# Optimization experiments

Hardware: AMD Instinct MI355X
Metric: run time of the kernel (lower is better)

The kernel has to match this reference:

```python
import jax, jax.numpy as jnp
import numpy as np

D_MODEL = 1024
N_HEADS = 16
D_HEAD = 64
BATCH = 4
SEQ = 2048
NEG = -1000000000.0


def setup_inputs() -> dict:
    key = jax.random.key(0)
    k1, k2, k3, k4, k5 = jax.random.split(key, 5)
    x = jax.random.normal(k1, (BATCH, SEQ, D_MODEL), dtype=jnp.float32)
    std = 0.02
    wq = jax.random.normal(k2, (N_HEADS, D_HEAD, D_MODEL), dtype=jnp.float32) * std
    wk = jax.random.normal(k3, (N_HEADS, D_HEAD, D_MODEL), dtype=jnp.float32) * std
    wv = jax.random.normal(k4, (N_HEADS, D_HEAD, D_MODEL), dtype=jnp.float32) * std
    wo = jax.random.normal(k5, (D_MODEL, N_HEADS * D_HEAD), dtype=jnp.float32) * std
    return {"x": x, "wq": wq, "wk": wk, "wv": wv, "wo": wo}


def reference(x, wq, wk, wv, wo):
    # x: [b, s, d_model]; wq/wk/wv: [h, d_head, d_model]; wo: [d_model, h*d_head]
    b, s, _ = x.shape
    scale = jnp.sqrt(jnp.asarray(D_HEAD, x.dtype))
    q = jnp.einsum('bsd,hed->bhse', x, wq)
    k = jnp.einsum('bsd,hed->bhse', x, wk)
    v = jnp.einsum('bsd,hed->bhse', x, wv)
    scores = jnp.einsum('bhse,bhte->bhst', q, k) / scale
    causal_mask = jnp.triu(jnp.ones((s, s), dtype=bool), k=1)
    scores = jnp.where(causal_mask, jnp.asarray(NEG, scores.dtype), scores)
    weights = jax.nn.softmax(scores, axis=-1)
    heads = jnp.einsum('bhst,bhte->bhse', weights, v)  # [b, h, s, d_head]
    concat = heads.transpose(0, 2, 1, 3).reshape(b, s, N_HEADS * D_HEAD)
    return concat @ wo.T
```

## Files before the change

kernel.cpp:

```cpp
#include <hip/hip_runtime.h>


#define DEV __device__ __forceinline__

typedef __attribute__((ext_vector_type(8))) __bf16 bf16x8;
typedef __attribute__((ext_vector_type(4))) float f32x4;
typedef unsigned short u16;

struct alignas(8) U16x4 { u16 x, y, z, w; };

DEV u16 f2bf(float f) {
  unsigned int u = __builtin_bit_cast(unsigned int, f);
  u = u + 0x7FFFu + ((u >> 16) & 1u);
  return (u16)(u >> 16);
}

DEV unsigned cvt_pk_bf16(float a, float b) {
  unsigned r;
  asm("v_cvt_pk_bf16_f32 %0, %1, %2" : "=v"(r) : "v"(a), "v"(b));
  return r;
}

DEV f32x4 mfma16(uint2 a, uint2 b, f32x4 c) {
  f32x4 d;
  asm("v_mfma_f32_16x16x16_bf16 %0, %1, %2, %3" : "=v"(d) : "v"(a), "v"(b), "v"(c));
  return d;
}

DEV void gload_lds16(const void* g, void* l) {
  __builtin_amdgcn_global_load_lds(
      (const __attribute__((address_space(1))) unsigned int*)g,
      (__attribute__((address_space(3))) unsigned int*)l, 16, 0, 0);
}

__global__ __launch_bounds__(256) void cast_all_kernel(
    const float* __restrict__ x, const float* __restrict__ wq,
    const float* __restrict__ wk, const float* __restrict__ wv,
    const float* __restrict__ wo, u16* __restrict__ xb,
    u16* __restrict__ wqkvb, u16* __restrict__ wob) {
  const int i = blockIdx.x * blockDim.x + threadIdx.x;
  const float* src;
  U16x4* dst;
  if (i < 2097152) {
    src = x + (size_t)i * 4;
    dst = reinterpret_cast<U16x4*>(xb) + i;
  } else if (i < 2883584) {
    const int j = i - 2097152;
    const int sel = j >> 18;
    const float* s = sel == 0 ? wq : sel == 1 ? wk : wv;
    src = s + (size_t)(j & 262143) * 4;
    dst = reinterpret_cast<U16x4*>(wqkvb) + j;
  } else {
    const int j = i - 2883584;
    src = wo + (size_t)j * 4;
    dst = reinterpret_cast<U16x4*>(wob) + j;
  }
  const float4 v = *reinterpret_cast<const float4*>(src);
  *dst = U16x4{f2bf(v.x), f2bf(v.y), f2bf(v.z), f2bf(v.w)};
}

template <int MODE, int NBN, bool SBUF>
__global__ __launch_bounds__(256, SBUF ? 3 : 2) void gemm_bt(
    const u16* __restrict__ A, const u16* __restrict__ B,
    void* __restrict__ C0, u16* __restrict__ vtp, int N) {
  constexpr int K = 1024;
  const int d = blockIdx.x;
  const int chunk = gridDim.x >> 3;
  const int vg = (d & 7) * chunk + (d >> 3);
  const int bn = vg % NBN, bm = vg / NBN;
  const int tid = threadIdx.x;
  const int w = tid >> 6, lane = tid & 63, lo = lane & 15, hi = lane >> 4;
  const int wm = w >> 1, wn = w & 1;

  __shared__ char lds[SBUF ? 32768 : 65536];
  char* sA = lds;
  char* sB = lds + (SBUF ? 16384 : 32768);

  const u16* Ag = A + (size_t)(bm * 128) * K;
  const u16* Bg = B + (size_t)(bn * 128) * K;

  f32x4 acc[4][4] = {};

  auto stage = [&](int buf, int k0) {
#pragma unroll
    for (int it = 0; it < 4; ++it) {
      const int L = (it * 4 + w) * 64 + lane;
      const int r = L >> 3, p = L & 7, c = p ^ (r & 7);
      gload_lds16(Ag + (size_t)r * K + k0 + c * 8, sA + buf * 16384 + (it * 4 + w) * 1024);
      gload_lds16(Bg + (size_t)r * K + k0 + c * 8, sB + buf * 16384 + (it * 4 + w) * 1024);
    }
  };
  auto compute = [&](int buf) {
#pragma unroll
    for (int kc = 0; kc < 2; ++kc) {
      bf16x8 af[4], bfr[4];
#pragma unroll
      for (int m = 0; m < 4; ++m) {
        const int r = wm * 64 + m * 16 + lo;
        const int p = (kc * 4 + hi) ^ (r & 7);
        af[m] = *reinterpret_cast<const bf16x8*>(sA + buf * 16384 + r * 128 + p * 16);
      }
#pragma unroll
      for (int n = 0; n < 4; ++n) {
        const int r = wn * 64 + n * 16 + lo;
        const int p = (kc * 4 + hi) ^ (r & 7);
        bfr[n] = *reinterpret_cast<const bf16x8*>(sB + buf * 16384 + r * 128 + p * 16);
      }
#pragma unroll
      for (int m = 0; m < 4; ++m)
#pragma unroll
        for (int n = 0; n < 4; ++n)
          acc[m][n] = __builtin_amdgcn_mfma_f32_16x16x32_bf16(af[m], bfr[n], acc[m][n], 0, 0, 0);
    }
  };

  if constexpr (SBUF) {
    for (int t = 0; t < 16; ++t) {
      stage(0, t * 64);
      __syncthreads();
      compute(0);
      __syncthreads();
    }
  } else {
    stage(0, 0);
    __syncthreads();
    int cur = 0;
    for (int t = 0; t < 16; ++t) {
      if (t + 1 < 16) stage(cur ^ 1, (t + 1) * 64);
      compute(cur);
      __syncthreads();
      cur ^= 1;
    }
  }

  const int colW = bn * 128 + wn * 64;
  const int rowW = bm * 128 + wm * 64;
  if (MODE == 0) {
    float* C = (float*)C0;
#pragma unroll
    for (int m = 0; m < 4; ++m)
#pragma unroll
      for (int n = 0; n < 4; ++n) {
        const int col = colW + n * 16 + lo;
        const int rb = rowW + m * 16 + hi * 4;
#pragma unroll
        for (int rg = 0; rg < 4; ++rg)
          C[(size_t)(rb + rg) * N + col] = acc[m][n][rg];
      }
  } else {
    u16* qkvp = (u16*)C0;
    if (bn * 128 < 2048) {
      const float qs = (bn < 8) ? 0.18033688011112042f : 1.0f;
#pragma unroll
      for (int m = 0; m < 4; ++m)
#pragma unroll
        for (int n = 0; n < 4; ++n) {
          const int col = colW + n * 16 + lo;
          const int rb = rowW + m * 16 + hi * 4;
#pragma unroll
          for (int rg = 0; rg < 4; ++rg)
            qkvp[(size_t)(rb + rg) * 2048 + col] = f2bf(acc[m][n][rg] * qs);
        }
    } else {
#pragma unroll
      for (int m = 0; m < 4; ++m)
#pragma unroll
        for (int n = 0; n < 4; ++n) {
          const int col = colW + n * 16 + lo;
          const int idx = col - 2048;
          const int hh = idx >> 6, e = idx & 63;
          const int rb = rowW + m * 16 + hi * 4;
          const int bb = rb >> 11, s = rb & 2047;
          U16x4 v4{f2bf(acc[m][n][0]), f2bf(acc[m][n][1]),
                   f2bf(acc[m][n][2]), f2bf(acc[m][n][3])};
          *reinterpret_cast<U16x4*>(vtp + ((size_t)((bb * 16 + hh) * 64 + e)) * 2048 + s) = v4;
        }
    }
  }
}

__global__ __launch_bounds__(512, 4) void attn_kernel(
    const u16* __restrict__ qkv, const u16* __restrict__ vt, u16* __restrict__ heads) {
  const int dd = blockIdx.x;
  const int vg = (dd & 7) * 64 + (dd >> 3);
  const int bx = vg & 7, bh = vg >> 3;
  const int b = bh >> 4, h = bh & 15;
  const int tid = threadIdx.x;
  const int w = tid >> 6, lane = tid & 63, lo = lane & 15, hi = lane >> 4;

  __shared__ char lds[81920];
  char* sQP = lds;
  char* sK  = lds + 16384;
  char* sV  = lds + 49152;

  const u16* Kg = qkv + (size_t)(b * 2048) * 2048 + 1024 + h * 64;
  const u16* Vg = vt + (size_t)bh * 64 * 2048;

  const int kr = tid >> 3, kc_ = (tid & 7) ^ (kr & 7);
  const int vr = tid >> 4, vc_ = (tid & 15) ^ (vr & 7);
  auto stageKV = [&](int buf, int kv0) {
#pragma unroll
    for (int it = 0; it < 2; ++it) {
      gload_lds16(Kg + (size_t)(kv0 + it * 64 + kr) * 2048 + kc_ * 8,
                  sK + buf * 16384 + it * 8192 + w * 1024);
      gload_lds16(Vg + (size_t)(it * 32 + vr) * 2048 + kv0 + vc_ * 8,
                  sV + buf * 16384 + it * 8192 + w * 1024);
    }
  };

  const int qloc = w * 16 + lo;

  for (int rep = 0; rep < 2; ++rep) {
    const int qt = rep ? (15 - bx) : bx;
    const u16* Qg = qkv + (size_t)(b * 2048 + qt * 128) * 2048 + h * 64;

#pragma unroll
    for (int it = 0; it < 2; ++it)
      gload_lds16(Qg + (size_t)(it * 64 + kr) * 2048 + kc_ * 8, sQP + it * 8192 + w * 1024);
    stageKV(0, 0);
    __syncthreads();

    bf16x8 qf[2];
#pragma unroll
    for (int kc = 0; kc < 2; ++kc) {
      const int p = (kc * 4 + hi) ^ (lo & 7);
      qf[kc] = *reinterpret_cast<const bf16x8*>(sQP + qloc * 128 + p * 16);
    }

    f32x4 lvec = {};
    f32x4 oacc[4] = {};

    const int nt = qt + 1;

    auto step = [&](int t, int cur) {
      if (t + 1 < nt) stageKV(cur ^ 1, (t + 1) * 128);
      f32x4 sa[8] = {};
      __builtin_amdgcn_s_setprio(1);
#pragma unroll
      for (int kc = 0; kc < 2; ++kc) {
#pragma unroll
        for (int n = 0; n < 8; ++n) {
          const int r = n * 16 + lo;
          const int p = (kc * 4 + hi) ^ (lo & 7);
          const bf16x8 kf = *reinterpret_cast<const bf16x8*>(sK + cur * 16384 + r * 128 + p * 16);
          sa[n] = __builtin_amdgcn_mfma_f32_16x16x32_bf16(kf, qf[kc], sa[n], 0, 0, 0);
        }
      }
      __builtin_amdgcn_s_setprio(0);

      if (t == nt - 1) {
#pragma unroll
        for (int n = 0; n < 8; ++n)
#pragma unroll
          for (int rg = 0; rg < 4; ++rg)
            if (n * 16 + hi * 4 + rg > qloc) sa[n][rg] = -1e9f;
      }

#pragma unroll
      for (int n = 0; n < 8; ++n)
#pragma unroll
        for (int rg = 0; rg < 4; ++rg) sa[n][rg] = exp2f(sa[n][rg]);
      lvec += ((sa[0] + sa[1]) + (sa[2] + sa[3])) + ((sa[4] + sa[5]) + (sa[6] + sa[7]));

      __builtin_amdgcn_s_setprio(1);
#pragma unroll
      for (int n = 0; n < 8; ++n) {
        const uint2 pb{cvt_pk_bf16(sa[n][0], sa[n][1]), cvt_pk_bf16(sa[n][2], sa[n][3])};
        const int sb = (((2 * n + (hi >> 1)) ^ (lo & 7)) << 4) + ((hi & 1) << 3);
#pragma unroll
        for (int ne = 0; ne < 4; ++ne) {
          const uint2 vf = *reinterpret_cast<const uint2*>(
              sV + cur * 16384 + (ne * 16 + lo) * 256 + sb);
          oacc[ne] = mfma16(vf, pb, oacc[ne]);
        }
      }
      __builtin_amdgcn_s_setprio(0);
      __syncthreads();
    };

    for (int i = 0; i < nt; i += 2) {
      step(i, 0);
      if (i + 1 < nt) step(i + 1, 1);
    }

    float lsum = (lvec[0] + lvec[1]) + (lvec[2] + lvec[3]);
    lsum += __shfl_xor(lsum, 16);
    lsum += __shfl_xor(lsum, 32);
    const float inv = 1.0f / lsum;
    const int q = qt * 128 + qloc;
    u16* dst = heads + (size_t)(b * 2048 + q) * 1024 + h * 64;
#pragma unroll
    for (int ne = 0; ne < 4; ++ne) {
      const unsigned r0 = cvt_pk_bf16(oacc[ne][0] * inv, oacc[ne][1] * inv);
      const unsigned r1 = cvt_pk_bf16(oacc[ne][2] * inv, oacc[ne][3] * inv);
      *reinterpret_cast<uint2*>(dst + ne * 16 + hi * 4) = uint2{r0, r1};
    }
  }
}

extern "C" void kernel_launch(void* const* d_in, const int* in_sizes, int n_in,
                              void* d_out, int out_size, void* d_ws, size_t ws_size,
                              hipStream_t stream) {
  const float* x  = (const float*)d_in[0];
  const float* wq = (const float*)d_in[1];
  const float* wk = (const float*)d_in[2];
  const float* wv = (const float*)d_in[3];
  const float* wo = (const float*)d_in[4];

  char* ws = (char*)d_ws;
  u16* xb    = (u16*)(ws);
  u16* wqkvb = (u16*)(ws + 16777216);
  u16* wob   = (u16*)(ws + 23068672);
  u16* qkv   = (u16*)(ws + 25165824);
  u16* vtp   = (u16*)(ws + 58720256);
  u16* heads = (u16*)(ws + 75497472);

  cast_all_kernel<<<12288, 256, 0, stream>>>(x, wq, wk, wv, wo, xb, wqkvb, wob);

  gemm_bt<1, 24, true><<<1536, 256, 0, stream>>>(xb, wqkvb, qkv, vtp, 3072);
  attn_kernel<<<512, 512, 0, stream>>>(qkv, vtp, heads);
  gemm_bt<0, 8, false><<<512, 256, 0, stream>>>(heads, wob, d_out, nullptr, 1024);
}
```

Before: 168.4 us.

## Restructure attention to 4 waves with 32 query rows each and 64-key tiles

The attention kernel goes from 8 waves of 16 query rows to 4 waves of 32 query rows, so each K/V fragment read from LDS feeds two MFMAs. KV tiles shrink from 128 to 64 keys, which cuts LDS to 48KB and lets each wave skip fully masked causal tiles. This lowers LDS read traffic per FLOP and wasted masked compute, at the cost of more registers per wave, fewer threads per block and twice as many barrier-separated steps.

After: 175.9 us. 4.5% more time.

```diff
diff --git a/kernel.cpp b/kernel.cpp
--- a/kernel.cpp
+++ b/kernel.cpp
@@ -179,7 +179,7 @@
   }
 }
 
-__global__ __launch_bounds__(512, 4) void attn_kernel(
+__global__ __launch_bounds__(256, 3) void attn_kernel(
     const u16* __restrict__ qkv, const u16* __restrict__ vt, u16* __restrict__ heads) {
   const int dd = blockIdx.x;
   const int vg = (dd & 7) * 64 + (dd >> 3);
@@ -188,112 +188,132 @@
   const int tid = threadIdx.x;
   const int w = tid >> 6, lane = tid & 63, lo = lane & 15, hi = lane >> 4;
 
-  __shared__ char lds[81920];
-  char* sQP = lds;
-  char* sK  = lds + 16384;
-  char* sV  = lds + 49152;
+  __shared__ char lds[49152];
+  char* sQ = lds;
+  char* sK = lds + 16384;
+  char* sV = lds + 32768;
 
   const u16* Kg = qkv + (size_t)(b * 2048) * 2048 + 1024 + h * 64;
   const u16* Vg = vt + (size_t)bh * 64 * 2048;
 
-  const int kr = tid >> 3, kc_ = (tid & 7) ^ (kr & 7);
-  const int vr = tid >> 4, vc_ = (tid & 15) ^ (vr & 7);
+  const int sr = lane >> 3, sc = (lane & 7) ^ (lane >> 3);
   auto stageKV = [&](int buf, int kv0) {
 #pragma unroll
-    for (int it = 0; it < 2; ++it) {
-      gload_lds16(Kg + (size_t)(kv0 + it * 64 + kr) * 2048 + kc_ * 8,
-                  sK + buf * 16384 + it * 8192 + w * 1024);
-      gload_lds16(Vg + (size_t)(it * 32 + vr) * 2048 + kv0 + vc_ * 8,
-                  sV + buf * 16384 + it * 8192 + w * 1024);
+    for (int rnd = 0; rnd < 2; ++rnd) {
+      const int r = rnd * 32 + w * 8 + sr;
+      gload_lds16(Kg + (size_t)(kv0 + r) * 2048 + sc * 8, sK + buf * 8192 + rnd * 4096 + w * 1024);
+      gload_lds16(Vg + (size_t)r * 2048 + kv0 + sc * 8, sV + buf * 8192 + rnd * 4096 + w * 1024);
     }
   };
 
-  const int qloc = w * 16 + lo;
+  const int qw = w * 32;
 
   for (int rep = 0; rep < 2; ++rep) {
     const int qt = rep ? (15 - bx) : bx;
     const u16* Qg = qkv + (size_t)(b * 2048 + qt * 128) * 2048 + h * 64;
 
 #pragma unroll
-    for (int it = 0; it < 2; ++it)
-      gload_lds16(Qg + (size_t)(it * 64 + kr) * 2048 + kc_ * 8, sQP + it * 8192 + w * 1024);
+    for (int it = 0; it < 4; ++it) {
+      const int r = it * 32 + w * 8 + sr;
+      gload_lds16(Qg + (size_t)r * 2048 + sc * 8, sQ + it * 4096 + w * 1024);
+    }
     stageKV(0, 0);
     __syncthreads();
 
-    bf16x8 qf[2];
-#pragma unroll
-    for (int kc = 0; kc < 2; ++kc) {
-      const int p = (kc * 4 + hi) ^ (lo & 7);
-      qf[kc] = *reinterpret_cast<const bf16x8*>(sQP + qloc * 128 + p * 16);
-    }
-
-    f32x4 lvec = {};
-    f32x4 oacc[4] = {};
-
-    const int nt = qt + 1;
+    bf16x8 qf[2][2];
+#pragma unroll
+    for (int qg = 0; qg < 2; ++qg)
+#pragma unroll
+      for (int kc = 0; kc < 2; ++kc) {
+        const int r = qw + qg * 16 + lo;
+        const int p = (kc * 4 + hi) ^ (lo & 7);
+        qf[qg][kc] = *reinterpret_cast<const bf16x8*>(sQ + r * 128 + p * 16);
+      }
+
+    f32x4 lvec[2] = {};
+    f32x4 oacc[2][4] = {};
+
+    const int nt = 2 * (qt + 1);
+    const int qmaxw = qt * 128 + qw + 31;
 
     auto step = [&](int t, int cur) {
-      if (t + 1 < nt) stageKV(cur ^ 1, (t + 1) * 128);
-      f32x4 sa[8] = {};
-      __builtin_amdgcn_s_setprio(1);
-#pragma unroll
-      for (int kc = 0; kc < 2; ++kc) {
-#pragma unroll
-        for (int n = 0; n < 8; ++n) {
-          const int r = n * 16 + lo;
-          const int p = (kc * 4 + hi) ^ (lo & 7);
-          const bf16x8 kf = *reinterpret_cast<const bf16x8*>(sK + cur * 16384 + r * 128 + p * 16);
-          sa[n] = __builtin_amdgcn_mfma_f32_16x16x32_bf16(kf, qf[kc], sa[n], 0, 0, 0);
-        }
-      }
-      __builtin_amdgcn_s_setprio(0);
-
-      if (t == nt - 1) {
-#pragma unroll
-        for (int n = 0; n < 8; ++n)
-#pragma unroll
-          for (int rg = 0; rg < 4; ++rg)
-            if (n * 16 + hi * 4 + rg > qloc) sa[n][rg] = -1e9f;
-      }
-
-#pragma unroll
-      for (int n = 0; n < 8; ++n)
-#pragma unroll
-        for (int rg = 0; rg < 4; ++rg) sa[n][rg] = exp2f(sa[n][rg]);
-      lvec += ((sa[0] + sa[1]) + (sa[2] + sa[3])) + ((sa[4] + sa[5]) + (sa[6] + sa[7]));
-
-      __builtin_amdgcn_s_setprio(1);
-#pragma unroll
-      for (int n = 0; n < 8; ++n) {
-        const uint2 pb{cvt_pk_bf16(sa[n][0], sa[n][1]), cvt_pk_bf16(sa[n][2], sa[n][3])};
-        const int sb = (((2 * n + (hi >> 1)) ^ (lo & 7)) << 4) + ((hi & 1) << 3);
-#pragma unroll
-        for (int ne = 0; ne < 4; ++ne) {
-          const uint2 vf = *reinterpret_cast<const uint2*>(
-              sV + cur * 16384 + (ne * 16 + lo) * 256 + sb);
-          oacc[ne] = mfma16(vf, pb, oacc[ne]);
-        }
-      }
-      __builtin_amdgcn_s_setprio(0);
+      if (t + 1 < nt) stageKV(cur ^ 1, (t + 1) * 64);
+      if (t * 64 <= qmaxw) {
+        f32x4 sa[2][4] = {};
+        __builtin_amdgcn_s_setprio(1);
+#pragma unroll
+        for (int kc = 0; kc < 2; ++kc) {
+#pragma unroll
+          for (int n = 0; n < 4; ++n) {
+            const int r = n * 16 + lo;
+            const int p = (kc * 4 + hi) ^ (lo & 7);
+            const bf16x8 kf = *reinterpret_cast<const bf16x8*>(sK + cur * 8192 + r * 128 + p * 16);
+            sa[0][n] = __builtin_amdgcn_mfma_f32_16x16x32_bf16(kf, qf[0][kc], sa[0][n], 0, 0, 0);
+            sa[1][n] = __builtin_amdgcn_mfma_f32_16x16x32_bf16(kf, qf[1][kc], sa[1][n], 0, 0, 0);
+          }
+        }
+        __builtin_amdgcn_s_setprio(0);
+
+        if (t >= nt - 2) {
+          const int kb = t * 64 - qt * 128;
+#pragma unroll
+          for (int qg = 0; qg < 2; ++qg) {
+            const int thr = qw + qg * 16 + lo - kb;
+#pragma unroll
+            for (int n = 0; n < 4; ++n)
+#pragma unroll
+              for (int rg = 0; rg < 4; ++rg)
+                if (n * 16 + hi * 4 + rg > thr) sa[qg][n][rg] = -1e9f;
+          }
+        }
+
+#pragma unroll
+        for (int qg = 0; qg < 2; ++qg) {
+#pragma unroll
+          for (int n = 0; n < 4; ++n)
+#pragma unroll
+            for (int rg = 0; rg < 4; ++rg) sa[qg][n][rg] = exp2f(sa[qg][n][rg]);
+          lvec[qg] += (sa[qg][0] + sa[qg][1]) + (sa[qg][2] + sa[qg][3]);
+        }
+
+        __builtin_amdgcn_s_setprio(1);
+#pragma unroll
+        for (int n = 0; n < 4; ++n) {
+          const uint2 pb0{cvt_pk_bf16(sa[0][n][0], sa[0][n][1]), cvt_pk_bf16(sa[0][n][2], sa[0][n][3])};
+          const uint2 pb1{cvt_pk_bf16(sa[1][n][0], sa[1][n][1]), cvt_pk_bf16(sa[1][n][2], sa[1][n][3])};
+          const int sb = (((2 * n + (hi >> 1)) ^ (lo & 7)) << 4) + ((hi & 1) << 3);
+#pragma unroll
+          for (int ne = 0; ne < 4; ++ne) {
+            const uint2 vf = *reinterpret_cast<const uint2*>(
+                sV + cur * 8192 + (ne * 16 + lo) * 128 + sb);
+            oacc[0][ne] = mfma16(vf, pb0, oacc[0][ne]);
+            oacc[1][ne] = mfma16(vf, pb1, oacc[1][ne]);
+          }
+        }
+        __builtin_amdgcn_s_setprio(0);
+      }
       __syncthreads();
     };
 
     for (int i = 0; i < nt; i += 2) {
       step(i, 0);
-      if (i + 1 < nt) step(i + 1, 1);
-    }
-
-    float lsum = (lvec[0] + lvec[1]) + (lvec[2] + lvec[3]);
-    lsum += __shfl_xor(lsum, 16);
-    lsum += __shfl_xor(lsum, 32);
-    const float inv = 1.0f / lsum;
-    const int q = qt * 128 + qloc;
-    u16* dst = heads + (size_t)(b * 2048 + q) * 1024 + h * 64;
-#pragma unroll
-    for (int ne = 0; ne < 4; ++ne) {
-      const unsigned r0 = cvt_pk_bf16(oacc[ne][0] * inv, oacc[ne][1] * inv);
-      const unsigned r1 = cvt_pk_bf16(oacc[ne][2] * inv, oacc[ne][3] * inv);
-      *reinterpret_cast<uint2*>(dst + ne * 16 + hi * 4) = uint2{r0, r1};
+      step(i + 1, 1);
+    }
+
+#pragma unroll
+    for (int qg = 0; qg < 2; ++qg) {
+      float lsum = (lvec[qg][0] + lvec[qg][1]) + (lvec[qg][2] + lvec[qg][3]);
+      lsum += __shfl_xor(lsum, 16);
+      lsum += __shfl_xor(lsum, 32);
+      const float inv = 1.0f / lsum;
+      const int q = qt * 128 + qw + qg * 16 + lo;
+      u16* dst = heads + (size_t)(b * 2048 + q) * 1024 + h * 64;
+#pragma unroll
+      for (int ne = 0; ne < 4; ++ne) {
+        const unsigned r0 = cvt_pk_bf16(oacc[qg][ne][0] * inv, oacc[qg][ne][1] * inv);
+        const unsigned r1 = cvt_pk_bf16(oacc[qg][ne][2] * inv, oacc[qg][ne][3] * inv);
+        *reinterpret_cast<uint2*>(dst + ne * 16 + hi * 4) = uint2{r0, r1};
+      }
     }
   }
 }
@@ -318,6 +338,6 @@
   cast_all_kernel<<<12288, 256, 0, stream>>>(x, wq, wk, wv, wo, xb, wqkvb, wob);
 
   gemm_bt<1, 24, true><<<1536, 256, 0, stream>>>(xb, wqkvb, qkv, vtp, 3072);
-  attn_kernel<<<512, 512, 0, stream>>>(qkv, vtp, heads);
+  attn_kernel<<<512, 256, 0, stream>>>(qkv, vtp, heads);
   gemm_bt<0, 8, false><<<512, 256, 0, stream>>>(heads, wob, d_out, nullptr, 1024);
 }
```

## Replace GEMM LDS staging with 4-deep K=32 ring buffer pipeline

Applied to the files above, without the earlier changes.

The GEMM kernel now stages 128x32 A/B tiles into a 4-slot LDS ring, prefetching three slices ahead. Explicit vmcnt waits and raw s_barrier replace __syncthreads, and MFMA issue gets raised priority. This replaces the single-buffer K=64 loop used by the QKV projection and the double buffer used by the output projection. The goal is to hide global-to-LDS latency behind MFMA work, at the cost of more barriers per K step and 64KB of LDS, which limits occupancy to 2 blocks.

Measured after the change: 169.6 us. Within noise of the previous version (+0.7%).

```diff
diff --git a/kernel.cpp b/kernel.cpp
--- a/kernel.cpp
+++ b/kernel.cpp
@@ -31,6 +31,13 @@
   __builtin_amdgcn_global_load_lds(
       (const __attribute__((address_space(1))) unsigned int*)g,
       (__attribute__((address_space(3))) unsigned int*)l, 16, 0, 0);
+}
+
+DEV void waitvm(int n) {
+  if (n >= 12)     asm volatile("s_waitcnt vmcnt(12)" ::: "memory");
+  else if (n == 8) asm volatile("s_waitcnt vmcnt(8)" ::: "memory");
+  else if (n == 4) asm volatile("s_waitcnt vmcnt(4)" ::: "memory");
+  else             asm volatile("s_waitcnt vmcnt(0)" ::: "memory");
 }
 
 __global__ __launch_bounds__(256) void cast_all_kernel(
@@ -59,8 +66,8 @@
   *dst = U16x4{f2bf(v.x), f2bf(v.y), f2bf(v.z), f2bf(v.w)};
 }
 
-template <int MODE, int NBN, bool SBUF>
-__global__ __launch_bounds__(256, SBUF ? 3 : 2) void gemm_bt(
+template <int MODE, int NBN>
+__global__ __launch_bounds__(256, 2) void gemm_bt(
     const u16* __restrict__ A, const u16* __restrict__ B,
     void* __restrict__ C0, u16* __restrict__ vtp, int N) {
   constexpr int K = 1024;
@@ -72,65 +79,57 @@
   const int w = tid >> 6, lane = tid & 63, lo = lane & 15, hi = lane >> 4;
   const int wm = w >> 1, wn = w & 1;
 
-  __shared__ char lds[SBUF ? 32768 : 65536];
-  char* sA = lds;
-  char* sB = lds + (SBUF ? 16384 : 32768);
+  __shared__ char lds[65536];
 
   const u16* Ag = A + (size_t)(bm * 128) * K;
   const u16* Bg = B + (size_t)(bn * 128) * K;
 
   f32x4 acc[4][4] = {};
 
-  auto stage = [&](int buf, int k0) {
-#pragma unroll
-    for (int it = 0; it < 4; ++it) {
-      const int L = (it * 4 + w) * 64 + lane;
-      const int r = L >> 3, p = L & 7, c = p ^ (r & 7);
-      gload_lds16(Ag + (size_t)r * K + k0 + c * 8, sA + buf * 16384 + (it * 4 + w) * 1024);
-      gload_lds16(Bg + (size_t)r * K + k0 + c * 8, sB + buf * 16384 + (it * 4 + w) * 1024);
+  auto stage = [&](int ring, int k0) {
+#pragma unroll
+    for (int j = 0; j < 2; ++j) {
+      const int L = j * 256 + tid, r = L >> 2, c = (L & 3) ^ (r & 3);
+      gload_lds16(Ag + (size_t)r * K + k0 + c * 8, lds + ring * 16384 + j * 4096 + w * 1024);
+      gload_lds16(Bg + (size_t)r * K + k0 + c * 8, lds + ring * 16384 + 8192 + j * 4096 + w * 1024);
     }
   };
-  auto compute = [&](int buf) {
-#pragma unroll
-    for (int kc = 0; kc < 2; ++kc) {
-      bf16x8 af[4], bfr[4];
-#pragma unroll
-      for (int m = 0; m < 4; ++m) {
-        const int r = wm * 64 + m * 16 + lo;
-        const int p = (kc * 4 + hi) ^ (r & 7);
-        af[m] = *reinterpret_cast<const bf16x8*>(sA + buf * 16384 + r * 128 + p * 16);
-      }
-#pragma unroll
-      for (int n = 0; n < 4; ++n) {
-        const int r = wn * 64 + n * 16 + lo;
-        const int p = (kc * 4 + hi) ^ (r & 7);
-        bfr[n] = *reinterpret_cast<const bf16x8*>(sB + buf * 16384 + r * 128 + p * 16);
-      }
-#pragma unroll
-      for (int m = 0; m < 4; ++m)
-#pragma unroll
-        for (int n = 0; n < 4; ++n)
-          acc[m][n] = __builtin_amdgcn_mfma_f32_16x16x32_bf16(af[m], bfr[n], acc[m][n], 0, 0, 0);
-    }
-  };
-
-  if constexpr (SBUF) {
-    for (int t = 0; t < 16; ++t) {
-      stage(0, t * 64);
-      __syncthreads();
-      compute(0);
-      __syncthreads();
-    }
-  } else {
-    stage(0, 0);
-    __syncthreads();
-    int cur = 0;
-    for (int t = 0; t < 16; ++t) {
-      if (t + 1 < 16) stage(cur ^ 1, (t + 1) * 64);
-      compute(cur);
-      __syncthreads();
-      cur ^= 1;
-    }
+
+  stage(0, 0);
+  stage(1, 32);
+  stage(2, 64);
+
+#pragma unroll
+  for (int t = 0; t < 32; ++t) {
+    if (t + 3 < 32) stage((t + 3) & 3, (t + 3) * 32);
+    waitvm(4 * (31 - t < 3 ? 31 - t : 3));
+    __builtin_amdgcn_sched_barrier(0);
+    __builtin_amdgcn_s_barrier();
+
+    const int ro = (t & 3) * 16384;
+    bf16x8 af[4], bfr[4];
+#pragma unroll
+    for (int m = 0; m < 4; ++m) {
+      const int r = wm * 64 + m * 16 + lo;
+      const int p = hi ^ (lo & 3);
+      af[m] = *reinterpret_cast<const bf16x8*>(lds + ro + r * 64 + p * 16);
+    }
+#pragma unroll
+    for (int n = 0; n < 4; ++n) {
+      const int r = wn * 64 + n * 16 + lo;
+      const int p = hi ^ (lo & 3);
+      bfr[n] = *reinterpret_cast<const bf16x8*>(lds + ro + 8192 + r * 64 + p * 16);
+    }
+    __builtin_amdgcn_s_setprio(1);
+#pragma unroll
+    for (int m = 0; m < 4; ++m)
+#pragma unroll
+      for (int n = 0; n < 4; ++n)
+        acc[m][n] = __builtin_amdgcn_mfma_f32_16x16x32_bf16(af[m], bfr[n], acc[m][n], 0, 0, 0);
+    __builtin_amdgcn_s_setprio(0);
+    asm volatile("s_waitcnt lgkmcnt(0)" ::: "memory");
+    __builtin_amdgcn_sched_barrier(0);
+    __builtin_amdgcn_s_barrier();
   }
 
   const int colW = bn * 128 + wn * 64;
@@ -317,7 +316,7 @@
 
   cast_all_kernel<<<12288, 256, 0, stream>>>(x, wq, wk, wv, wo, xb, wqkvb, wob);
 
-  gemm_bt<1, 24, true><<<1536, 256, 0, stream>>>(xb, wqkvb, qkv, vtp, 3072);
+  gemm_bt<1, 24><<<1536, 256, 0, stream>>>(xb, wqkvb, qkv, vtp, 3072);
   attn_kernel<<<512, 512, 0, stream>>>(qkv, vtp, heads);
-  gemm_bt<0, 8, false><<<512, 256, 0, stream>>>(heads, wob, d_out, nullptr, 1024);
-}
+  gemm_bt<0, 8><<<512, 256, 0, stream>>>(heads, wob, d_out, nullptr, 1024);
+}
```
